# Kernel optimization log

Measured on AMD Instinct MI355X. Metric: run time of the kernel, lower is better.

The kernel has to match this reference:

```python
import jax, jax.numpy as jnp
import numpy as np

H = 256      # hidden_dim
NH = 8       # num_heads
D = H // NH  # per-head dim
NEG = -(2.0**32) + 1.0
EPS = 1e-5


def setup_inputs() -> dict:
    key = jax.random.key(0)
    ks = jax.random.split(key, 12)
    N, Tq, Tk = 2, 2048, 2048
    s = 1.0 / np.sqrt(H)
    return {
        "Q": jax.random.normal(ks[0], (N, Tq, H), jnp.float32),
        "K": jax.random.normal(ks[1], (N, Tk, H), jnp.float32),
        "V": jax.random.normal(ks[2], (N, Tk, H), jnp.float32),
        "Wq": jax.random.normal(ks[3], (H, H), jnp.float32) * s,
        "bq": jnp.zeros((H,), jnp.float32),
        "Wk": jax.random.normal(ks[4], (H, H), jnp.float32) * s,
        "bk": jnp.zeros((H,), jnp.float32),
        "Wv": jax.random.normal(ks[5], (H, H), jnp.float32) * s,
        "bv": jnp.zeros((H,), jnp.float32),
        "gamma": jnp.ones((H,), jnp.float32),
        "beta": jnp.zeros((H,), jnp.float32),
    }


def _split_heads(x):
    # [N,T,H] -> [h,N,T,D]  (matches torch split(dim=2)+cat(dim=0): head-major)
    N, T, _ = x.shape
    return x.reshape(N, T, NH, D).transpose(2, 0, 1, 3)


def reference(Q, K, V, Wq, bq, Wk, bk, Wv, bv, gamma, beta):
    N, Tq, _ = Q.shape
    Tk = K.shape[1]
    Ql = jax.nn.relu(Q @ Wq + bq)
    Kl = jax.nn.relu(K @ Wk + bk)
    Vl = jax.nn.relu(V @ Wv + bv)
    Qh, Kh, Vh = _split_heads(Ql), _split_heads(Kl), _split_heads(Vl)

    scores = jnp.einsum("hnqd,hnkd->hnqk", Qh, Kh) / jnp.sqrt(jnp.float32(D))
    key_mask = jnp.sign(jnp.abs(K).sum(-1))    # [N,Tk]
    scores = jnp.where(key_mask[None, :, None, :] == 0, NEG, scores)
    attn = jax.nn.softmax(scores / 0.01, axis=-1)
    query_mask = jnp.sign(jnp.abs(Q).sum(-1))  # [N,Tq]
    attn = attn * query_mask[None, :, :, None]  # dropout p=0 -> identity

    ctx = jnp.einsum("hnqk,hnkd->hnqd", attn[..., :-1], Vh[:, :, :-1, :])
    out = ctx.transpose(1, 2, 0, 3).reshape(N, Tq, H)

    mu = out.mean(-1, keepdims=True)
    var = ((out - mu) ** 2).mean(-1, keepdims=True)
    out = (out - mu) / jnp.sqrt(var + EPS) * gamma + beta

    weight = attn.transpose(1, 2, 0, 3).reshape(N, Tq, NH * Tk).mean(-1)
    return out, weight
```

## Files before the change

kernel.cpp:

```cpp
#include <hip/hip_runtime.h>
#include <math.h>

#define H_DIM 256
#define NHEAD 8
#define DHEAD 32
#define NB 2
#define TSEQ 2048
#define LN_EPS 1e-5f

#define QK2_SCALE 25.503486f
#define NEG2 (-6.2e11f)

typedef _Float16 half8 __attribute__((ext_vector_type(8)));
typedef float f32x4 __attribute__((ext_vector_type(4)));

__device__ __forceinline__ f32x4 mfma16(half8 a, half8 b, f32x4 c) {
  return __builtin_amdgcn_mfma_f32_16x16x32_f16(a, b, c, 0, 0, 0);
}
__device__ __forceinline__ float exp2fast(float x) {
  return __builtin_amdgcn_exp2f(x);
}

__global__ __launch_bounds__(256) void mask_kernel(
    const float* __restrict__ Q, const float* __restrict__ K,
    float* __restrict__ qmask, float* __restrict__ kmask) {
  const int wid = threadIdx.x >> 6, lane = threadIdx.x & 63;
  int row = blockIdx.x * 4 + wid;
  const int total_q = NB * TSEQ;
  const float* src;
  float* dst;
  if (row < total_q) { src = Q + (size_t)row * H_DIM; dst = qmask + row; }
  else               { src = K + (size_t)(row - total_q) * H_DIM; dst = kmask + (row - total_q); }
  float4 v = *(const float4*)(src + lane * 4);
  float s = fabsf(v.x) + fabsf(v.y) + fabsf(v.z) + fabsf(v.w);
  #pragma unroll
  for (int off = 32; off > 0; off >>= 1) s += __shfl_xor(s, off);
  if (lane == 0) *dst = (s != 0.0f) ? 1.0f : 0.0f;
}

__global__ __launch_bounds__(256) void prepack_kernel(
    const float* __restrict__ Wq, const float* __restrict__ Wk, const float* __restrict__ Wv,
    half8* __restrict__ WpkHi, half8* __restrict__ WpkLo) {
  int slot = blockIdx.x * 256 + threadIdx.x;
  int lane = slot & 63;
  int fg = (slot >> 6) & 15;
  int s  = (slot >> 10) & 7;
  int which = slot >> 13;
  const float* W = which == 0 ? Wq : which == 1 ? Wk : Wv;
  int j  = fg * 16 + (lane & 15);
  int kb = s * 32 + (lane >> 4) * 8;
  half8 hi, lo;
  #pragma unroll
  for (int jj = 0; jj < 8; ++jj) {
    float x = W[(size_t)(kb + jj) * H_DIM + j];
    _Float16 h = (_Float16)x;
    hi[jj] = h;
    lo[jj] = (_Float16)(x - (float)h);
  }
  WpkHi[slot] = hi;
  WpkLo[slot] = lo;
}

__global__ __launch_bounds__(256) void proj_kernel(
    const float* __restrict__ Q, const float* __restrict__ K, const float* __restrict__ V,
    const float* __restrict__ bq, const float* __restrict__ bk, const float* __restrict__ bv,
    const half8* __restrict__ WpkHi, const half8* __restrict__ WpkLo,
    float* __restrict__ Qh, float* __restrict__ Kh, float* __restrict__ Vh) {
  const int which = blockIdx.z;
  const float* X    = which == 0 ? Q  : which == 1 ? K  : V;
  const float* bias = which == 0 ? bq : which == 1 ? bk : bv;
  float* dst        = which == 0 ? Qh : which == 1 ? Kh : Vh;

  const int tid = threadIdx.x;
  const int w = tid >> 6, lane = tid & 63;
  const int l15 = lane & 15, quad = lane >> 4;
  const int mbase = blockIdx.y * 64;
  const int nfg   = blockIdx.x * 4;

  half8 ahi[8], alo[8];
  {
    const float* xrow = X + (size_t)(mbase + w * 16 + l15) * H_DIM + quad * 8;
    #pragma unroll
    for (int s = 0; s < 8; ++s) {
      float4 a0 = *(const float4*)(xrow + s * 32);
      float4 a1 = *(const float4*)(xrow + s * 32 + 4);
      float xs[8] = {a0.x, a0.y, a0.z, a0.w, a1.x, a1.y, a1.z, a1.w};
      #pragma unroll
      for (int i = 0; i < 8; ++i) {
        _Float16 h = (_Float16)xs[i];
        ahi[s][i] = h;
        alo[s][i] = (_Float16)(xs[i] - (float)h);
      }
    }
  }

  f32x4 acc[4];
  #pragma unroll
  for (int f = 0; f < 4; ++f) acc[f] = (f32x4){0.f, 0.f, 0.f, 0.f};

  #pragma unroll
  for (int s = 0; s < 8; ++s) {
    const half8* ph = WpkHi + (((size_t)which * 8 + s) * 16 + nfg) * 64 + lane;
    const half8* pl = WpkLo + (((size_t)which * 8 + s) * 16 + nfg) * 64 + lane;
    #pragma unroll
    for (int f = 0; f < 4; ++f) {
      half8 BH = ph[f * 64];
      half8 BL = pl[f * 64];
      acc[f] = mfma16(ahi[s], BH, acc[f]);
      acc[f] = mfma16(ahi[s], BL, acc[f]);
      acc[f] = mfma16(alo[s], BH, acc[f]);
    }
  }

  #pragma unroll
  for (int f = 0; f < 4; ++f) {
    int j = blockIdx.x * 64 + f * 16 + l15;
    float bj = bias[j];
    int hh = j >> 5, dd = j & 31;
    #pragma unroll
    for (int r = 0; r < 4; ++r) {
      int m = mbase + w * 16 + quad * 4 + r;
      int n = m >> 11, t = m & (TSEQ - 1);
      float val = fmaxf(acc[f][r] + bj, 0.0f);
      if (which == 2 && t == TSEQ - 1) val = 0.0f;
      dst[(((size_t)hh * NB + n) * TSEQ + t) * DHEAD + dd] = val;
    }
  }
}

__global__ __launch_bounds__(256) void attn_kernel(
    const float* __restrict__ Qh, const float* __restrict__ Kh, const float* __restrict__ Vh,
    const float* __restrict__ kmask,
    float* __restrict__ Op, float* __restrict__ Mp, float* __restrict__ Lp) {
  __shared__ __align__(16) half8 KfH[256];
  __shared__ __align__(16) half8 KfL[256];
  __shared__ __align__(16) half8 Vf[256];
  __shared__ __align__(16) _Float16 Pbuf[4][16][72];

  const int tid = threadIdx.x;
  const int w = tid >> 6, lane = tid & 63;
  const int l15 = lane & 15, quad = lane >> 4;

  const int b = blockIdx.x;
  const int g    = ((b & 7) << 1) | ((b >> 3) & 1);
  const int qt   = (b >> 4) & 31;
  const int sblk = b >> 9;
  const int h = g >> 1, n = g & 1;

  const float* Qbase = Qh + ((size_t)h * NB + n) * TSEQ * DHEAD;
  const float* Kbase = Kh + ((size_t)h * NB + n) * TSEQ * DHEAD;
  const float* Vbase = Vh + ((size_t)h * NB + n) * TSEQ * DHEAD;
  const float* kmp   = kmask + (size_t)n * TSEQ;
  const int qbase  = qt * 64;
  const int kstart = sblk * 1024;

  half8 qhi, qlo;
  {
    const float* qp = Qbase + (size_t)(qbase + w * 16 + l15) * DHEAD + quad * 8;
    #pragma unroll
    for (int i = 0; i < 8; ++i) {
      float x = qp[i];
      _Float16 hi = (_Float16)x;
      qhi[i] = hi;
      qlo[i] = (_Float16)(x - (float)hi);
    }
  }

  half8 onesb;
  #pragma unroll
  for (int i = 0; i < 8; ++i) onesb[i] = (l15 == 0) ? (_Float16)1.0f : (_Float16)0.0f;

  float m_r[4];
  f32x4 O0, O1, Ol;
  #pragma unroll
  for (int r = 0; r < 4; ++r) m_r[r] = -1.0e38f;
  O0 = (f32x4){0.f, 0.f, 0.f, 0.f};
  O1 = (f32x4){0.f, 0.f, 0.f, 0.f};
  Ol = (f32x4){0.f, 0.f, 0.f, 0.f};

  const int kr = tid >> 2, kdc = tid & 3;
  const int vd = tid & 31, vkg = tid >> 5;

  for (int kt = kstart; kt < kstart + 1024; kt += 64) {
    __syncthreads();
    {
      const float* kp = Kbase + (size_t)(kt + kr) * DHEAD + kdc * 8;
      half8 hi8, lo8;
      #pragma unroll
      for (int i = 0; i < 8; ++i) {
        float x = kp[i];
        _Float16 hi = (_Float16)x;
        hi8[i] = hi;
        lo8[i] = (_Float16)(x - (float)hi);
      }
      int kslot = ((kr >> 4) << 6) | (kdc << 4) | (kr & 15);
      KfH[kslot] = hi8;
      KfL[kslot] = lo8;
      const float* vp = Vbase + (size_t)(kt + vkg * 8) * DHEAD + vd;
      half8 v8;
      #pragma unroll
      for (int j = 0; j < 8; ++j) v8[j] = (_Float16)vp[j * DHEAD];
      int vslot = (((vkg >> 2) << 1) | (vd >> 4)) << 6 | ((vkg & 3) << 4) | (vd & 15);
      Vf[vslot] = v8;
    }
    __syncthreads();

    f32x4 S[4];
    #pragma unroll
    for (int f = 0; f < 4; ++f) {
      half8 bh = KfH[(f << 6) | lane];
      half8 bl = KfL[(f << 6) | lane];
      f32x4 a = (f32x4){0.f, 0.f, 0.f, 0.f};
      a = mfma16(qhi, bh, a);
      a = mfma16(qhi, bl, a);
      a = mfma16(qlo, bh, a);
      S[f] = a;
    }
    float kmf[4];
    #pragma unroll
    for (int f = 0; f < 4; ++f) kmf[f] = kmp[kt + (f << 4) + l15];

    float lg[4][4];
    #pragma unroll
    for (int r = 0; r < 4; ++r)
      #pragma unroll
      for (int f = 0; f < 4; ++f)
        lg[r][f] = (kmf[f] != 0.0f) ? S[f][r] * QK2_SCALE : NEG2;

    float mx[4];
    #pragma unroll
    for (int r = 0; r < 4; ++r)
      mx[r] = fmaxf(fmaxf(lg[r][0], lg[r][1]), fmaxf(lg[r][2], lg[r][3]));
    #pragma unroll
    for (int off = 1; off < 16; off <<= 1) {
      #pragma unroll
      for (int r = 0; r < 4; ++r) mx[r] = fmaxf(mx[r], __shfl_xor(mx[r], off));
    }
    float alpha[4];
    #pragma unroll
    for (int r = 0; r < 4; ++r) {
      float mnew = fmaxf(m_r[r], mx[r]);
      alpha[r] = exp2fast(m_r[r] - mnew);
      m_r[r] = mnew;
    }
    #pragma unroll
    for (int r = 0; r < 4; ++r) {
      int row = (quad << 2) + r;
      #pragma unroll
      for (int f = 0; f < 4; ++f) {
        float p = exp2fast(lg[r][f] - m_r[r]);
        Pbuf[w][row][(f << 4) + l15] = (_Float16)p;
      }
    }
    #pragma unroll
    for (int r = 0; r < 4; ++r) {
      O0[r] *= alpha[r];
      O1[r] *= alpha[r];
      Ol[r] *= alpha[r];
    }
    asm volatile("s_waitcnt lgkmcnt(0)" ::: "memory");

    #pragma unroll
    for (int c = 0; c < 2; ++c) {
      half8 pa = *(const half8*)&Pbuf[w][l15][(c << 5) + (quad << 3)];
      O0 = mfma16(pa, Vf[((c << 1) | 0) << 6 | lane], O0);
      O1 = mfma16(pa, Vf[((c << 1) | 1) << 6 | lane], O1);
      Ol = mfma16(pa, onesb, Ol);
    }
  }

  #pragma unroll
  for (int r = 0; r < 4; ++r) {
    int q = qbase + w * 16 + (quad << 2) + r;
    size_t idx = ((size_t)(sblk * 16 + g) * TSEQ + q) * DHEAD;
    Op[idx + l15]      = O0[r];
    Op[idx + 16 + l15] = O1[r];
    if (l15 == 0) {
      Mp[(size_t)(sblk * 16 + g) * TSEQ + q] = m_r[r];
      Lp[(size_t)(sblk * 16 + g) * TSEQ + q] = Ol[r];
    }
  }
}

__global__ __launch_bounds__(256) void ln_kernel(
    const float* __restrict__ Op, const float* __restrict__ Mp, const float* __restrict__ Lp,
    const float* __restrict__ gamma, const float* __restrict__ beta,
    const float* __restrict__ qmask,
    float* __restrict__ out, float* __restrict__ wout) {
  const int wid = threadIdx.x >> 6, lane = threadIdx.x & 63;
  const int row = blockIdx.x * 4 + wid;
  const int n = row >> 11, q = row & (TSEQ - 1);
  const int hh = lane >> 3;
  const int hn = hh * NB + n;
  const int dbase = (lane & 7) * 4;

  size_t i1 = ((size_t)(0 * 16 + hn) * TSEQ + q) * DHEAD + dbase;
  size_t i2 = ((size_t)(1 * 16 + hn) * TSEQ + q) * DHEAD + dbase;
  float4 P1 = *(const float4*)(Op + i1);
  float4 P2 = *(const float4*)(Op + i2);
  size_t s1 = (size_t)(0 * 16 + hn) * TSEQ + q;
  size_t s2 = (size_t)(1 * 16 + hn) * TSEQ + q;
  float m1 = Mp[s1], m2 = Mp[s2];
  float l1 = Lp[s1], l2 = Lp[s2];
  float mm = fmaxf(m1, m2);
  float a1 = exp2fast(m1 - mm), a2 = exp2fast(m2 - mm);
  float qm = qmask[row];
  float inv = qm / (l1 * a1 + l2 * a2);

  float4 x;
  x.x = (P1.x * a1 + P2.x * a2) * inv;
  x.y = (P1.y * a1 + P2.y * a2) * inv;
  x.z = (P1.z * a1 + P2.z * a2) * inv;
  x.w = (P1.w * a1 + P2.w * a2) * inv;

  float s = x.x + x.y + x.z + x.w;
  #pragma unroll
  for (int off = 32; off > 0; off >>= 1) s += __shfl_xor(s, off);
  float mu = s * (1.0f / H_DIM);
  float dx0 = x.x - mu, dx1 = x.y - mu, dx2 = x.z - mu, dx3 = x.w - mu;
  float sq = dx0 * dx0 + dx1 * dx1 + dx2 * dx2 + dx3 * dx3;
  #pragma unroll
  for (int off = 32; off > 0; off >>= 1) sq += __shfl_xor(sq, off);
  float rstd = rsqrtf(sq * (1.0f / H_DIM) + LN_EPS);
  float4 g = *(const float4*)(gamma + lane * 4);
  float4 bb = *(const float4*)(beta + lane * 4);
  float4 y;
  y.x = dx0 * rstd * g.x + bb.x;
  y.y = dx1 * rstd * g.y + bb.y;
  y.z = dx2 * rstd * g.z + bb.z;
  y.w = dx3 * rstd * g.w + bb.w;
  *(float4*)(out + (size_t)row * H_DIM + lane * 4) = y;
  if (lane == 0) wout[row] = qm * (1.0f / TSEQ);
}

extern "C" void kernel_launch(void* const* d_in, const int* in_sizes, int n_in,
                              void* d_out, int out_size, void* d_ws, size_t ws_size,
                              hipStream_t stream) {
  const float* Q  = (const float*)d_in[0];
  const float* K  = (const float*)d_in[1];
  const float* V  = (const float*)d_in[2];
  const float* Wq = (const float*)d_in[3];
  const float* bq = (const float*)d_in[4];
  const float* Wk = (const float*)d_in[5];
  const float* bk = (const float*)d_in[6];
  const float* Wv = (const float*)d_in[7];
  const float* bv = (const float*)d_in[8];
  const float* gamma = (const float*)d_in[9];
  const float* beta  = (const float*)d_in[10];

  float* ws = (float*)d_ws;
  const size_t per = (size_t)NHEAD * NB * TSEQ * DHEAD;
  float* Qh = ws;
  float* Kh = Qh + per;
  float* Vh = Kh + per;
  float* Opart = Vh + per;
  float* Mp = Opart + 2 * per;
  float* Lp = Mp + 2 * 16 * TSEQ;
  float* qmask = Lp + 2 * 16 * TSEQ;
  float* kmask = qmask + NB * TSEQ;
  half8* WpkHi = (half8*)(kmask + NB * TSEQ);
  half8* WpkLo = WpkHi + 3 * 8 * 16 * 64;

  float* out  = (float*)d_out;
  float* wout = out + (size_t)NB * TSEQ * H_DIM;

  hipLaunchKernelGGL(mask_kernel, dim3(2 * NB * TSEQ / 4), dim3(256), 0, stream,
                     Q, K, qmask, kmask);
  hipLaunchKernelGGL(prepack_kernel, dim3(96), dim3(256), 0, stream,
                     Wq, Wk, Wv, WpkHi, WpkLo);
  hipLaunchKernelGGL(proj_kernel, dim3(H_DIM / 64, NB * TSEQ / 64, 3), dim3(256), 0, stream,
                     Q, K, V, bq, bk, bv, WpkHi, WpkLo, Qh, Kh, Vh);
  hipLaunchKernelGGL(attn_kernel, dim3(NHEAD * NB * (TSEQ / 64) * 2), dim3(256), 0, stream,
                     Qh, Kh, Vh, kmask, Opart, Mp, Lp);
  hipLaunchKernelGGL(ln_kernel, dim3(NB * TSEQ / 4), dim3(256), 0, stream,
                     Opart, Mp, Lp, gamma, beta, qmask, out, wout);
}
```

Before: 153.4 us.

## Pre-split Q/K/V into MFMA fragments, raise key split to four, double-buffer V

Adds a repack kernel that converts the projected Q, K and V once into fp16 hi/lo MFMA fragment layouts, with the softmax scale folded into Q. The attention kernel then reads K fragments directly from global memory, double-buffers only V in shared memory, and removes the per-tile fp32-to-fp16 conversion and one barrier. The key dimension is split four ways instead of two for more blocks, and the row max uses DPP instead of shuffles. The LN kernel merges four partials. This costs an extra launch, extra workspace traffic, and aliases Opart onto the Qh/Kh/Vh workspace.

```diff
diff --git a/kernel.cpp b/kernel.cpp
--- a/kernel.cpp
+++ b/kernel.cpp
@@ -10,6 +10,8 @@
 
 #define QK2_SCALE 25.503486f
 #define NEG2 (-6.2e11f)
+#define SPLIT 4
+#define TILES_PER (TSEQ / 64 / SPLIT)
 
 typedef _Float16 half8 __attribute__((ext_vector_type(8)));
 typedef float f32x4 __attribute__((ext_vector_type(4)));
@@ -20,6 +22,15 @@
 __device__ __forceinline__ float exp2fast(float x) {
   return __builtin_amdgcn_exp2f(x);
 }
+#define DPP_MAX4(mx, CTRL)                                                   \
+  {                                                                          \
+    _Pragma("unroll")                                                        \
+    for (int r = 0; r < 4; ++r) {                                            \
+      int t_ = __builtin_amdgcn_update_dpp(0, __float_as_int(mx[r]), CTRL,   \
+                                           0xf, 0xf, false);                 \
+      mx[r] = fmaxf(mx[r], __int_as_float(t_));                              \
+    }                                                                        \
+  }
 
 __global__ __launch_bounds__(256) void mask_kernel(
     const float* __restrict__ Q, const float* __restrict__ K,
@@ -128,13 +139,53 @@
   }
 }
 
+__global__ __launch_bounds__(256) void repack_kernel(
+    const float* __restrict__ Qh, const float* __restrict__ Kh, const float* __restrict__ Vh,
+    half8* __restrict__ Gqhi, half8* __restrict__ Gqlo,
+    half8* __restrict__ Gkhi, half8* __restrict__ Gklo, half8* __restrict__ Gv) {
+  const int tile = blockIdx.x;
+  const int hn   = blockIdx.y;
+  const int which = blockIdx.z;
+  const int tid = threadIdx.x;
+  if (which < 2) {
+    const int w = tid >> 6, lane = tid & 63;
+    const int f = w, krlo = lane >> 2, kdc = lane & 3;
+    const float* src = (which == 0 ? Qh : Kh) +
+        ((size_t)hn * TSEQ + tile * 64 + f * 16 + krlo) * DHEAD + kdc * 8;
+    float4 a0 = *(const float4*)src;
+    float4 a1 = *(const float4*)(src + 4);
+    float xs[8] = {a0.x, a0.y, a0.z, a0.w, a1.x, a1.y, a1.z, a1.w};
+    const float sc = which == 0 ? QK2_SCALE : 1.0f;
+    half8 hi, lo;
+    #pragma unroll
+    for (int i = 0; i < 8; ++i) {
+      float x = xs[i] * sc;
+      _Float16 h = (_Float16)x;
+      hi[i] = h;
+      lo[i] = (_Float16)(x - (float)h);
+    }
+    size_t di = ((size_t)hn * 32 + tile) * 256 + f * 64 + kdc * 16 + krlo;
+    if (which == 0) { Gqhi[di] = hi; Gqlo[di] = lo; }
+    else            { Gkhi[di] = hi; Gklo[di] = lo; }
+  } else {
+    const int s = tid;
+    const int top = s >> 6, mid = (s >> 4) & 3, low = s & 15;
+    const int c = top >> 1, hh = top & 1;
+    const int vkg = c * 4 + mid, vd = hh * 16 + low;
+    const float* src = Vh + ((size_t)hn * TSEQ + tile * 64 + vkg * 8) * DHEAD + vd;
+    half8 v8;
+    #pragma unroll
+    for (int j = 0; j < 8; ++j) v8[j] = (_Float16)src[j * DHEAD];
+    Gv[((size_t)hn * 32 + tile) * 256 + s] = v8;
+  }
+}
+
 __global__ __launch_bounds__(256) void attn_kernel(
-    const float* __restrict__ Qh, const float* __restrict__ Kh, const float* __restrict__ Vh,
-    const float* __restrict__ kmask,
+    const half8* __restrict__ Gqhi, const half8* __restrict__ Gqlo,
+    const half8* __restrict__ Gkhi, const half8* __restrict__ Gklo,
+    const half8* __restrict__ Gv, const float* __restrict__ kmask,
     float* __restrict__ Op, float* __restrict__ Mp, float* __restrict__ Lp) {
-  __shared__ __align__(16) half8 KfH[256];
-  __shared__ __align__(16) half8 KfL[256];
-  __shared__ __align__(16) half8 Vf[256];
+  __shared__ __align__(16) half8 Vf[2][256];
   __shared__ __align__(16) _Float16 Pbuf[4][16][72];
 
   const int tid = threadIdx.x;
@@ -145,26 +196,15 @@
   const int g    = ((b & 7) << 1) | ((b >> 3) & 1);
   const int qt   = (b >> 4) & 31;
   const int sblk = b >> 9;
-  const int h = g >> 1, n = g & 1;
-
-  const float* Qbase = Qh + ((size_t)h * NB + n) * TSEQ * DHEAD;
-  const float* Kbase = Kh + ((size_t)h * NB + n) * TSEQ * DHEAD;
-  const float* Vbase = Vh + ((size_t)h * NB + n) * TSEQ * DHEAD;
-  const float* kmp   = kmask + (size_t)n * TSEQ;
-  const int qbase  = qt * 64;
-  const int kstart = sblk * 1024;
-
-  half8 qhi, qlo;
-  {
-    const float* qp = Qbase + (size_t)(qbase + w * 16 + l15) * DHEAD + quad * 8;
-    #pragma unroll
-    for (int i = 0; i < 8; ++i) {
-      float x = qp[i];
-      _Float16 hi = (_Float16)x;
-      qhi[i] = hi;
-      qlo[i] = (_Float16)(x - (float)hi);
-    }
-  }
+  const int n = g & 1;
+
+  const size_t fbase = (size_t)g * 32 * 256;
+  const int tile0 = sblk * TILES_PER;
+
+  half8 qhi = Gqhi[fbase + (size_t)qt * 256 + w * 64 + lane];
+  half8 qlo = Gqlo[fbase + (size_t)qt * 256 + w * 64 + lane];
+
+  const float* kmp = kmask + (size_t)n * TSEQ + sblk * (TSEQ / SPLIT);
 
   half8 onesb;
   #pragma unroll
@@ -178,64 +218,52 @@
   O1 = (f32x4){0.f, 0.f, 0.f, 0.f};
   Ol = (f32x4){0.f, 0.f, 0.f, 0.f};
 
-  const int kr = tid >> 2, kdc = tid & 3;
-  const int vd = tid & 31, vkg = tid >> 5;
-
-  for (int kt = kstart; kt < kstart + 1024; kt += 64) {
+  {
+    half8 v0 = Gv[fbase + (size_t)tile0 * 256 + tid];
+    Vf[0][tid] = v0;
+  }
+
+  for (int tt = 0; tt < TILES_PER; ++tt) {
+    half8 vnext;
+    if (tt < TILES_PER - 1)
+      vnext = Gv[fbase + (size_t)(tile0 + tt + 1) * 256 + tid];
     __syncthreads();
-    {
-      const float* kp = Kbase + (size_t)(kt + kr) * DHEAD + kdc * 8;
-      half8 hi8, lo8;
-      #pragma unroll
-      for (int i = 0; i < 8; ++i) {
-        float x = kp[i];
-        _Float16 hi = (_Float16)x;
-        hi8[i] = hi;
-        lo8[i] = (_Float16)(x - (float)hi);
-      }
-      int kslot = ((kr >> 4) << 6) | (kdc << 4) | (kr & 15);
-      KfH[kslot] = hi8;
-      KfL[kslot] = lo8;
-      const float* vp = Vbase + (size_t)(kt + vkg * 8) * DHEAD + vd;
-      half8 v8;
-      #pragma unroll
-      for (int j = 0; j < 8; ++j) v8[j] = (_Float16)vp[j * DHEAD];
-      int vslot = (((vkg >> 2) << 1) | (vd >> 4)) << 6 | ((vkg & 3) << 4) | (vd & 15);
-      Vf[vslot] = v8;
-    }
-    __syncthreads();
-
+    if (tt < TILES_PER - 1)
+      Vf[(tt + 1) & 1][tid] = vnext;
+
+    const half8* kh = Gkhi + fbase + (size_t)(tile0 + tt) * 256;
+    const half8* kl = Gklo + fbase + (size_t)(tile0 + tt) * 256;
     f32x4 S[4];
     #pragma unroll
     for (int f = 0; f < 4; ++f) {
-      half8 bh = KfH[(f << 6) | lane];
-      half8 bl = KfL[(f << 6) | lane];
+      half8 KH = kh[f * 64 + lane];
+      half8 KL = kl[f * 64 + lane];
       f32x4 a = (f32x4){0.f, 0.f, 0.f, 0.f};
-      a = mfma16(qhi, bh, a);
-      a = mfma16(qhi, bl, a);
-      a = mfma16(qlo, bh, a);
+      a = mfma16(qlo, KH, a);
+      a = mfma16(qhi, KL, a);
+      a = mfma16(qhi, KH, a);
       S[f] = a;
     }
     float kmf[4];
     #pragma unroll
-    for (int f = 0; f < 4; ++f) kmf[f] = kmp[kt + (f << 4) + l15];
+    for (int f = 0; f < 4; ++f) kmf[f] = kmp[tt * 64 + (f << 4) + l15];
 
     float lg[4][4];
     #pragma unroll
     for (int r = 0; r < 4; ++r)
       #pragma unroll
       for (int f = 0; f < 4; ++f)
-        lg[r][f] = (kmf[f] != 0.0f) ? S[f][r] * QK2_SCALE : NEG2;
+        lg[r][f] = (kmf[f] != 0.0f) ? S[f][r] : NEG2;
 
     float mx[4];
     #pragma unroll
     for (int r = 0; r < 4; ++r)
       mx[r] = fmaxf(fmaxf(lg[r][0], lg[r][1]), fmaxf(lg[r][2], lg[r][3]));
-    #pragma unroll
-    for (int off = 1; off < 16; off <<= 1) {
-      #pragma unroll
-      for (int r = 0; r < 4; ++r) mx[r] = fmaxf(mx[r], __shfl_xor(mx[r], off));
-    }
+    DPP_MAX4(mx, 0x128);
+    DPP_MAX4(mx, 0x124);
+    DPP_MAX4(mx, 0x122);
+    DPP_MAX4(mx, 0x121);
+
     float alpha[4];
     #pragma unroll
     for (int r = 0; r < 4; ++r) {
@@ -247,10 +275,8 @@
     for (int r = 0; r < 4; ++r) {
       int row = (quad << 2) + r;
       #pragma unroll
-      for (int f = 0; f < 4; ++f) {
-        float p = exp2fast(lg[r][f] - m_r[r]);
-        Pbuf[w][row][(f << 4) + l15] = (_Float16)p;
-      }
+      for (int f = 0; f < 4; ++f)
+        Pbuf[w][row][(f << 4) + l15] = (_Float16)exp2fast(lg[r][f] - m_r[r]);
     }
     #pragma unroll
     for (int r = 0; r < 4; ++r) {
@@ -260,18 +286,19 @@
     }
     asm volatile("s_waitcnt lgkmcnt(0)" ::: "memory");
 
+    const half8* vbuf = (const half8*)Vf[tt & 1];
     #pragma unroll
     for (int c = 0; c < 2; ++c) {
       half8 pa = *(const half8*)&Pbuf[w][l15][(c << 5) + (quad << 3)];
-      O0 = mfma16(pa, Vf[((c << 1) | 0) << 6 | lane], O0);
-      O1 = mfma16(pa, Vf[((c << 1) | 1) << 6 | lane], O1);
+      O0 = mfma16(pa, vbuf[((c << 1) | 0) * 64 + lane], O0);
+      O1 = mfma16(pa, vbuf[((c << 1) | 1) * 64 + lane], O1);
       Ol = mfma16(pa, onesb, Ol);
     }
   }
 
   #pragma unroll
   for (int r = 0; r < 4; ++r) {
-    int q = qbase + w * 16 + (quad << 2) + r;
+    int q = qt * 64 + w * 16 + (quad << 2) + r;
     size_t idx = ((size_t)(sblk * 16 + g) * TSEQ + q) * DHEAD;
     Op[idx + l15]      = O0[r];
     Op[idx + 16 + l15] = O1[r];
@@ -294,24 +321,30 @@
   const int hn = hh * NB + n;
   const int dbase = (lane & 7) * 4;
 
-  size_t i1 = ((size_t)(0 * 16 + hn) * TSEQ + q) * DHEAD + dbase;
-  size_t i2 = ((size_t)(1 * 16 + hn) * TSEQ + q) * DHEAD + dbase;
-  float4 P1 = *(const float4*)(Op + i1);
-  float4 P2 = *(const float4*)(Op + i2);
-  size_t s1 = (size_t)(0 * 16 + hn) * TSEQ + q;
-  size_t s2 = (size_t)(1 * 16 + hn) * TSEQ + q;
-  float m1 = Mp[s1], m2 = Mp[s2];
-  float l1 = Lp[s1], l2 = Lp[s2];
-  float mm = fmaxf(m1, m2);
-  float a1 = exp2fast(m1 - mm), a2 = exp2fast(m2 - mm);
+  float4 P[SPLIT];
+  float m[SPLIT], l[SPLIT];
+  #pragma unroll
+  for (int i = 0; i < SPLIT; ++i) {
+    size_t si = (size_t)(i * 16 + hn) * TSEQ + q;
+    P[i] = *(const float4*)(Op + si * DHEAD + dbase);
+    m[i] = Mp[si];
+    l[i] = Lp[si];
+  }
+  float mm = fmaxf(fmaxf(m[0], m[1]), fmaxf(m[2], m[3]));
+  float denom = 0.f;
+  float a[SPLIT];
+  #pragma unroll
+  for (int i = 0; i < SPLIT; ++i) { a[i] = exp2fast(m[i] - mm); denom += l[i] * a[i]; }
   float qm = qmask[row];
-  float inv = qm / (l1 * a1 + l2 * a2);
-
-  float4 x;
-  x.x = (P1.x * a1 + P2.x * a2) * inv;
-  x.y = (P1.y * a1 + P2.y * a2) * inv;
-  x.z = (P1.z * a1 + P2.z * a2) * inv;
-  x.w = (P1.w * a1 + P2.w * a2) * inv;
+  float inv = qm / denom;
+
+  float4 x = make_float4(0.f, 0.f, 0.f, 0.f);
+  #pragma unroll
+  for (int i = 0; i < SPLIT; ++i) {
+    x.x += P[i].x * a[i]; x.y += P[i].y * a[i];
+    x.z += P[i].z * a[i]; x.w += P[i].w * a[i];
+  }
+  x.x *= inv; x.y *= inv; x.z *= inv; x.w *= inv;
 
   float s = x.x + x.y + x.z + x.w;
   #pragma unroll
@@ -349,17 +382,24 @@
   const float* beta  = (const float*)d_in[10];
 
   float* ws = (float*)d_ws;
-  const size_t per = (size_t)NHEAD * NB * TSEQ * DHEAD;
+  const size_t perHN = (size_t)16 * TSEQ * DHEAD;
   float* Qh = ws;
-  float* Kh = Qh + per;
-  float* Vh = Kh + per;
-  float* Opart = Vh + per;
-  float* Mp = Opart + 2 * per;
-  float* Lp = Mp + 2 * 16 * TSEQ;
-  float* qmask = Lp + 2 * 16 * TSEQ;
+  float* Kh = Qh + perHN;
+  float* Vh = Kh + perHN;
+  float* Opart = ws;
+  float* tail = ws + 4 * perHN;
+  const size_t NFRAG = (size_t)16 * 32 * 256;
+  half8* Gqhi = (half8*)tail;
+  half8* Gqlo = Gqhi + NFRAG;
+  half8* Gkhi = Gqlo + NFRAG;
+  half8* Gklo = Gkhi + NFRAG;
+  half8* Gv   = Gklo + NFRAG;
+  float* Mp = (float*)(Gv + NFRAG);
+  float* Lp = Mp + SPLIT * 16 * TSEQ;
+  float* qmask = Lp + SPLIT * 16 * TSEQ;
   float* kmask = qmask + NB * TSEQ;
   half8* WpkHi = (half8*)(kmask + NB * TSEQ);
-  half8* WpkLo = WpkHi + 3 * 8 * 16 * 64;
+  half8* WpkLo = WpkHi + 24576;
 
   float* out  = (float*)d_out;
   float* wout = out + (size_t)NB * TSEQ * H_DIM;
@@ -370,8 +410,10 @@
                      Wq, Wk, Wv, WpkHi, WpkLo);
   hipLaunchKernelGGL(proj_kernel, dim3(H_DIM / 64, NB * TSEQ / 64, 3), dim3(256), 0, stream,
                      Q, K, V, bq, bk, bv, WpkHi, WpkLo, Qh, Kh, Vh);
-  hipLaunchKernelGGL(attn_kernel, dim3(NHEAD * NB * (TSEQ / 64) * 2), dim3(256), 0, stream,
-                     Qh, Kh, Vh, kmask, Opart, Mp, Lp);
+  hipLaunchKernelGGL(repack_kernel, dim3(32, 16, 3), dim3(256), 0, stream,
+                     Qh, Kh, Vh, Gqhi, Gqlo, Gkhi, Gklo, Gv);
+  hipLaunchKernelGGL(attn_kernel, dim3(16 * 32 * SPLIT), dim3(256), 0, stream,
+                     Gqhi, Gqlo, Gkhi, Gklo, Gv, kmask, Opart, Mp, Lp);
   hipLaunchKernelGGL(ln_kernel, dim3(NB * TSEQ / 4), dim3(256), 0, stream,
                      Opart, Mp, Lp, gamma, beta, qmask, out, wout);
 }
```

Result: no change. 151.5 us (-1.2%).
